# Performance work log

Measured on AMD Instinct MI355X. Metric: run time of the kernel, lower is better.

The kernel has to match this reference:

```python
import jax, jax.numpy as jnp
import numpy as np

B, N, Q, D = 1, 6, 10000, 256
HEADS, LEVELS, NPTS, ZANCH = 8, 1, 8, 4  # NPTS = 2*n_points, ZANCH = num_points_in_pillar
HF, WF = 32, 88
HD = D // HEADS


def setup_inputs() -> dict:
    key = jax.random.key(0)
    ks = jax.random.split(key, 18)
    s = 1.0 / np.sqrt(D)
    inp = {
        'queries': jax.random.normal(ks[0], (B, N, Q, D), jnp.float32),
        'pos_emb': jax.random.normal(ks[1], (B, N, Q, D), jnp.float32),
        'lvl_emb': jax.random.normal(ks[2], (LEVELS, D), jnp.float32),
        'cam_emb': jax.random.normal(ks[3], (N, D), jnp.float32),
        'features0': jax.random.normal(ks[4], (B * N, D, HF, WF), jnp.float32),
        'reference_points_3D': jax.random.uniform(ks[5], (B, N, Q, ZANCH, 2), jnp.float32),
        'bev_mask': jax.random.randint(ks[6], (B, N, Q, ZANCH, 2), 0, 2).astype(bool),
        # MSDeformAttn3D params
        'W_value': jax.random.normal(ks[7], (D, D), jnp.float32) * s,
        'b_value': jnp.zeros((D,), jnp.float32),
        'W_off': jax.random.normal(ks[8], (HEADS * LEVELS * NPTS * 2, D), jnp.float32) * 0.01,
        'b_off': jax.random.uniform(ks[9], (HEADS * LEVELS * NPTS * 2,), jnp.float32, -2.0, 2.0),
        'W_attn': jax.random.normal(ks[10], (HEADS * LEVELS * NPTS, D), jnp.float32) * s,
        'b_attn': jnp.zeros((HEADS * LEVELS * NPTS,), jnp.float32),
        'W_inner': jax.random.normal(ks[11], (D, D), jnp.float32) * s,
        'b_inner': jnp.zeros((D,), jnp.float32),
        # SpatialCrossAttention.output_proj
        'W_out': jax.random.normal(ks[12], (D, D), jnp.float32) * s,
        'b_out': jnp.zeros((D,), jnp.float32),
    }
    return inp


def _bilinear(value_t, loc, H, W):
    # value_t: (bn, heads, H*W, hd); loc: (bn, q, heads, pts, 2) normalized to [0,1]
    bn, q, heads, pts, _ = loc.shape
    hd = value_t.shape[-1]
    # grid_sample(2*loc-1, align_corners=False) -> pixel coord = loc*size - 0.5
    x = loc[..., 0] * W - 0.5
    y = loc[..., 1] * H - 0.5
    x0 = jnp.floor(x); y0 = jnp.floor(y)
    dx = x - x0; dy = y - y0
    x0 = x0.astype(jnp.int32); y0 = y0.astype(jnp.int32)
    out = jnp.zeros((bn, heads, q * pts, hd), value_t.dtype)
    corners = ((0, 0, (1 - dx) * (1 - dy)), (1, 0, dx * (1 - dy)),
               (0, 1, (1 - dx) * dy), (1, 1, dx * dy))
    for ox, oy, w in corners:
        xi = x0 + ox; yi = y0 + oy
        valid = (xi >= 0) & (xi < W) & (yi >= 0) & (yi < H)  # zero padding
        wgt = jnp.where(valid, w, 0.0)
        idx = jnp.clip(yi, 0, H - 1) * W + jnp.clip(xi, 0, W - 1)  # (bn,q,heads,pts)
        idx_t = idx.transpose(0, 2, 1, 3).reshape(bn, heads, q * pts)
        g = jnp.take_along_axis(value_t, idx_t[..., None], axis=2)  # (bn,heads,q*pts,hd)
        wgt_t = wgt.transpose(0, 2, 1, 3).reshape(bn, heads, q * pts)
        out = out + g * wgt_t[..., None]
    return out.reshape(bn, heads, q, pts, hd)


def _forward(queries, pos_emb, lvl_emb, cam_emb, features0, reference_points_3D, bev_mask,
             W_value, b_value, W_off, b_off, W_attn, b_attn, W_inner, b_inner, W_out, b_out):
    b, n, q, d = queries.shape
    hf, wf = features0.shape[-2:]
    # flatten features + level/cam embeddings -> (b*n, hw, d)
    feat = features0.reshape(b, n, d, hf * wf)
    feat = feat + lvl_emb[0][None, None, :, None] + cam_emb[None, :, :, None]
    input_flatten = feat.transpose(0, 1, 3, 2).reshape(b * n, hf * wf, d)

    qp = (queries + pos_emb).reshape(b * n, q, d)
    ref = reference_points_3D.reshape(b * n, q, ZANCH, 2)

    # --- MSDeformAttn3D (single level) ---
    value = (input_flatten @ W_value.T + b_value).reshape(b * n, hf * wf, HEADS, HD)
    off = (qp @ W_off.T + b_off).reshape(b * n, q, HEADS, LEVELS, NPTS, 2)
    attw = jax.nn.softmax((qp @ W_attn.T + b_attn).reshape(b * n, q, HEADS, LEVELS * NPTS), axis=-1)
    attw = attw.reshape(b * n, q, HEADS, LEVELS, NPTS)
    normalizer = jnp.array([wf, hf], queries.dtype)  # (W, H)
    pts_per_z = NPTS // ZANCH
    off_z = off.reshape(b * n, q, HEADS, LEVELS, pts_per_z, ZANCH, 2)
    loc = ref[:, :, None, None, None, :, :] + off_z / normalizer
    loc = loc.reshape(b * n, q, HEADS, LEVELS, NPTS, 2)

    value_t = value.transpose(0, 2, 1, 3)  # (bn, heads, hw, hd)
    sampled = _bilinear(value_t, loc[:, :, :, 0], hf, wf)  # (bn,heads,q,pts,hd)
    attw_t = attw[:, :, :, 0].transpose(0, 2, 1, 3)  # (bn,heads,q,pts)
    out = jnp.einsum('bhqp,bhqpc->bqhc', attw_t, sampled).reshape(b * n, q, d)
    out = out @ W_inner.T + b_inner

    # --- scatter back per camera, normalize by hit count ---
    attn = out.reshape(b, n, q, d)
    # indexes come from batch 0's mask (as in the original code)
    hit = (bev_mask[0, :, :, :, 0].astype(jnp.int32).sum(-1) > 0).astype(queries.dtype)  # (n,q)
    slots = (attn * hit[None, :, :, None]).sum(1)  # (b,q,d)
    count = (bev_mask[..., 0].astype(jnp.int32).sum(-1) > 0).astype(queries.dtype).sum(1)
    count = jnp.clip(count, 1.0, None)  # (b,q)
    slots = slots / count[..., None]
    return slots @ W_out.T + b_out


def reference(queries, pos_emb, lvl_emb, cam_emb, features0, reference_points_3D, bev_mask,
              W_value, b_value, W_off, b_off, W_attn, b_attn, W_inner, b_inner, W_out, b_out):
    return _forward(queries, pos_emb, lvl_emb, cam_emb, features0, reference_points_3D, bev_mask,
                    W_value, b_value, W_off, b_off, W_attn, b_attn, W_inner, b_inner, W_out, b_out)
```

## Files before the change

### kernel.cpp

```cpp
#include <hip/hip_runtime.h>
#include <hip/hip_bf16.h>

#define BN     6
#define NQ     10000
#define DIM    256
#define HEADS  8
#define HDD    32
#define HF_    32
#define WF_    88
#define HW_    (HF_*WF_)
#define MTOT   (BN*NQ)

typedef __attribute__((ext_vector_type(8))) unsigned short ushort8_t;
typedef __attribute__((ext_vector_type(8))) short bf16x8;
typedef __attribute__((ext_vector_type(4))) float f32x4;

static __device__ inline unsigned short f2bf(float x) {
    __hip_bfloat16 b = __float2bfloat16(x);
    return *(unsigned short*)&b;
}

__global__ __launch_bounds__(256)
void k_wcvt(const float* __restrict__ Wv, const float* __restrict__ Wo,
            const float* __restrict__ Wa, const float* __restrict__ Wi,
            const float* __restrict__ Wz,
            unsigned short* __restrict__ Wv_bf, unsigned short* __restrict__ Woa_bf,
            unsigned short* __restrict__ Wi_bf, unsigned short* __restrict__ Wz_bf)
{
    const int i4 = (blockIdx.x*256 + threadIdx.x) * 4;
    if (i4 < 65536) {
        float4 v;
        ushort4 p;
        v = *(const float4*)(Wv+i4); p.x=f2bf(v.x);p.y=f2bf(v.y);p.z=f2bf(v.z);p.w=f2bf(v.w);
        *(ushort4*)(Wv_bf+i4) = p;
        v = *(const float4*)(Wi+i4); p.x=f2bf(v.x);p.y=f2bf(v.y);p.z=f2bf(v.z);p.w=f2bf(v.w);
        *(ushort4*)(Wi_bf+i4) = p;
        v = *(const float4*)(Wz+i4); p.x=f2bf(v.x);p.y=f2bf(v.y);p.z=f2bf(v.z);p.w=f2bf(v.w);
        *(ushort4*)(Wz_bf+i4) = p;
    }
    if (i4 < 32768) {
        float4 v = *(const float4*)(Wo+i4);
        ushort4 p; p.x=f2bf(v.x);p.y=f2bf(v.y);p.z=f2bf(v.z);p.w=f2bf(v.w);
        *(ushort4*)(Woa_bf+i4) = p;
    }
    if (i4 < 16384) {
        float4 v = *(const float4*)(Wa+i4);
        ushort4 p; p.x=f2bf(v.x);p.y=f2bf(v.y);p.z=f2bf(v.z);p.w=f2bf(v.w);
        *(ushort4*)(Woa_bf+32768+i4) = p;
    }
}

__global__ __launch_bounds__(256)
void k_ebias(const float* __restrict__ lvl, const float* __restrict__ cam,
             const float* __restrict__ Wv, const float* __restrict__ bv,
             float* __restrict__ ebias)
{
    const int n = blockIdx.x;
    const int j = threadIdx.x;
    __shared__ float e[DIM];
    e[j] = lvl[j] + cam[n*DIM + j];
    __syncthreads();
    const float* w = Wv + (size_t)j*DIM;
    float s = bv[j];
    for (int d = 0; d < DIM; ++d) s += e[d]*w[d];
    ebias[n*DIM + j] = s;
}

__global__ __launch_bounds__(256)
void k_mask(const int* __restrict__ bev, float* __restrict__ hitf,
            float* __restrict__ scale, float* __restrict__ biasf)
{
    const int q = blockIdx.x*256 + threadIdx.x;
    if (q >= NQ) return;
    float cnt = 0.f;
    #pragma unroll
    for (int n = 0; n < BN; ++n) {
        int hit = 0;
        #pragma unroll
        for (int z = 0; z < 4; ++z)
            hit |= (bev[(((size_t)n*NQ + q)*4 + z)*2] != 0);
        hitf[(size_t)n*NQ + q] = (float)hit;
        cnt += (float)hit;
    }
    biasf[q] = (cnt > 0.f) ? 1.f : 0.f;
    scale[q] = 1.f / fmaxf(cnt, 1.f);
}

__global__ __launch_bounds__(256)
void k_feat(const float* __restrict__ feat, unsigned short* __restrict__ featT)
{
    __shared__ float Tf[64][68];
    const int cam = blockIdx.z;
    const int d0 = blockIdx.y * 64;
    const int p0 = blockIdx.x * 64;
    const int tid = threadIdx.x;
    #pragma unroll
    for (int i = 0; i < 4; ++i) {
        const int d = (tid>>4) + i*16;
        const int p4 = (tid&15)*4;
        *(float4*)&Tf[d][p4] = *(const float4*)(feat + ((size_t)cam*DIM + d0 + d)*HW_ + p0 + p4);
    }
    __syncthreads();
    const int p = tid>>2, dq = tid&3;
    unsigned short* ob = featT + ((size_t)cam*HW_ + p0 + p)*DIM + d0;
    #pragma unroll
    for (int i = 0; i < 4; ++i) {
        const int d4 = dq*4 + i*16;
        ushort4 pk;
        pk.x = f2bf(Tf[d4+0][p]); pk.y = f2bf(Tf[d4+1][p]);
        pk.z = f2bf(Tf[d4+2][p]); pk.w = f2bf(Tf[d4+3][p]);
        *(ushort4*)(ob + d4) = pk;
    }
}

__global__ __launch_bounds__(256)
void k_value_mfma(const unsigned short* __restrict__ featT,
                  const unsigned short* __restrict__ Wv_bf,
                  const float* __restrict__ ebias,
                  unsigned short* __restrict__ value_bf)
{
    __shared__ unsigned short Ap[128][72];
    __shared__ unsigned short Bc[64][72];
    const int cam = blockIdx.z;
    const int p0 = blockIdx.x * 128;
    const int c0 = blockIdx.y * 64;
    const int tid = threadIdx.x;
    const int lane = tid & 63, wave = tid >> 6;
    const int quad = lane >> 4, l15 = lane & 15;
    f32x4 acc[2][4] = {};
    const unsigned short* fbase = featT + ((size_t)cam*HW_ + p0)*DIM;

    for (int k0 = 0; k0 < DIM; k0 += 64) {
        #pragma unroll
        for (int i = 0; i < 4; ++i) {
            const int row = (tid>>3) + i*32;
            const int k8 = (tid&7)*8;
            *(ushort8_t*)&Ap[row][k8] = *(const ushort8_t*)(fbase + (size_t)row*DIM + k0 + k8);
        }
        #pragma unroll
        for (int i = 0; i < 2; ++i) {
            const int row = (tid>>3) + i*32;
            const int k8 = (tid&7)*8;
            *(ushort8_t*)&Bc[row][k8] = *(const ushort8_t*)(Wv_bf + (size_t)(c0+row)*DIM + k0 + k8);
        }
        __syncthreads();
        #pragma unroll
        for (int s = 0; s < 2; ++s) {
            const int kf = s*32 + quad*8;
            bf16x8 a[2], b[4];
            #pragma unroll
            for (int mt = 0; mt < 2; ++mt)
                a[mt] = *(const bf16x8*)&Ap[(wave*2+mt)*16 + l15][kf];
            #pragma unroll
            for (int nt = 0; nt < 4; ++nt)
                b[nt] = *(const bf16x8*)&Bc[nt*16 + l15][kf];
            #pragma unroll
            for (int mt = 0; mt < 2; ++mt)
                #pragma unroll
                for (int nt = 0; nt < 4; ++nt)
                    acc[mt][nt] = __builtin_amdgcn_mfma_f32_16x16x32_bf16(a[mt], b[nt], acc[mt][nt], 0,0,0);
        }
        __syncthreads();
    }
    #pragma unroll
    for (int nt = 0; nt < 4; ++nt) {
        const int c = c0 + nt*16 + l15;
        const float eb = ebias[cam*DIM + c];
        const int h = c >> 5, cc = c & 31;
        unsigned short* vb = value_bf + (size_t)(cam*HEADS + h)*HW_*HDD + cc;
        #pragma unroll
        for (int mt = 0; mt < 2; ++mt)
            #pragma unroll
            for (int r = 0; r < 4; ++r) {
                const int p = p0 + (wave*2+mt)*16 + quad*4 + r;
                vb[(size_t)p*HDD] = f2bf(acc[mt][nt][r] + eb);
            }
    }
}

__global__ __launch_bounds__(256, 3)
void k_offattn(const float* __restrict__ Qr, const float* __restrict__ Pe,
               const unsigned short* __restrict__ Woa_bf,
               const float* __restrict__ boff, const float* __restrict__ battn,
               float* __restrict__ off_ws, float* __restrict__ attw_ws)
{
    __shared__ char smraw[32*204*4];
    unsigned short (*A_lds)[264] = (unsigned short (*)[264])smraw;
    float (*C_lds)[204] = (float (*)[204])smraw;

    const int m0 = blockIdx.x * 32;
    const int tid = threadIdx.x;
    const int lane = tid & 63, wave = tid >> 6;
    const int quad = lane >> 4, l15 = lane & 15;
    const int n0 = wave * 48;

    bf16x8 breg[3][8];
    #pragma unroll
    for (int nt = 0; nt < 3; ++nt) {
        const unsigned short* wb = Woa_bf + (size_t)(n0 + nt*16 + l15)*DIM + quad*8;
        #pragma unroll
        for (int kc = 0; kc < 8; ++kc)
            breg[nt][kc] = *(const bf16x8*)(wb + kc*32);
    }

    {
        const int row = tid >> 3;
        const int c8  = tid & 7;
        const float* qb = Qr + (size_t)(m0 + row)*DIM;
        const float* pb = Pe + (size_t)(m0 + row)*DIM;
        #pragma unroll
        for (int j = 0; j < 8; ++j) {
            const int col = c8*4 + j*32;
            const float4 x = *(const float4*)(qb + col);
            const float4 y = *(const float4*)(pb + col);
            ushort4 pk;
            pk.x = f2bf(x.x+y.x); pk.y = f2bf(x.y+y.y);
            pk.z = f2bf(x.z+y.z); pk.w = f2bf(x.w+y.w);
            *(ushort4*)&A_lds[row][col] = pk;
        }
    }
    __syncthreads();

    f32x4 acc[2][3] = {};
    #pragma unroll
    for (int kc = 0; kc < 8; ++kc) {
        const int kk = kc*32 + quad*8;
        const bf16x8 a0 = *(const bf16x8*)&A_lds[l15][kk];
        const bf16x8 a1 = *(const bf16x8*)&A_lds[16 + l15][kk];
        #pragma unroll
        for (int nt = 0; nt < 3; ++nt) {
            acc[0][nt] = __builtin_amdgcn_mfma_f32_16x16x32_bf16(a0, breg[nt][kc], acc[0][nt], 0,0,0);
            acc[1][nt] = __builtin_amdgcn_mfma_f32_16x16x32_bf16(a1, breg[nt][kc], acc[1][nt], 0,0,0);
        }
    }

    __syncthreads();
    #pragma unroll
    for (int nt = 0; nt < 3; ++nt) {
        const int col = n0 + nt*16 + l15;
        const float bias = (col < 128) ? boff[col] : battn[col-128];
        #pragma unroll
        for (int mt = 0; mt < 2; ++mt) {
            #pragma unroll
            for (int r = 0; r < 4; ++r)
                C_lds[mt*16 + quad*4 + r][col] = acc[mt][nt][r] + bias;
        }
    }
    __syncthreads();
    #pragma unroll
    for (int i = 0; i < 4; ++i) {
        const int idx = i*256 + tid;
        const int row = idx >> 5, c4 = (idx & 31)*4;
        *(float4*)(off_ws + ((size_t)(m0+row))*128 + c4) = *(float4*)&C_lds[row][c4];
    }
    #pragma unroll
    for (int i = 0; i < 2; ++i) {
        const int idx = i*256 + tid;
        const int row = idx >> 4, c4 = (idx & 15)*4;
        *(float4*)(attw_ws + ((size_t)(m0+row))*64 + c4) = *(float4*)&C_lds[row][128 + c4];
    }
}

__global__ __launch_bounds__(256)
void k_sample(const unsigned short* __restrict__ value_bf,
              const float* __restrict__ off_ws, const float* __restrict__ attw_ws,
              const float* __restrict__ ref3d, const float* __restrict__ hitf,
              const float* __restrict__ scale, unsigned short* __restrict__ asum_bf)
{
    const int q0 = blockIdx.x * 8;
    const int tid = threadIdx.x;

    __shared__ float s_off[8][128];
    __shared__ float s_att[8][64];
    __shared__ float s_ref[8][8];
    __shared__ float s_hit[BN][8];
    __shared__ float s_scl[8];

    if (tid < 48) s_hit[tid>>3][tid&7] = hitf[(size_t)(tid>>3)*NQ + q0 + (tid&7)];
    if (tid < 8)  s_scl[tid] = scale[q0 + tid];

    const int quarter = tid & 3;
    const int h  = (tid >> 2) & 7;
    const int ql = tid >> 5;

    float acc[8];
    #pragma unroll
    for (int c = 0; c < 8; ++c) acc[c] = 0.f;

    for (int n = 0; n < BN; ++n) {
        __syncthreads();
        {
            const float4* so = (const float4*)(off_ws + ((size_t)n*NQ + q0)*128);
            ((float4*)&s_off[0][0])[tid] = so[tid];
            const float2* sa = (const float2*)(attw_ws + ((size_t)n*NQ + q0)*64);
            ((float2*)&s_att[0][0])[tid] = sa[tid];
            if (tid < 64)
                (&s_ref[0][0])[tid] = (ref3d + ((size_t)n*NQ + q0)*8)[tid];
        }
        __syncthreads();

        if (s_hit[n][ql] != 0.f) {
            float lg[8];
            float mx = -1e30f;
            #pragma unroll
            for (int p = 0; p < 8; ++p) { lg[p] = s_att[ql][h*8+p]; mx = fmaxf(mx, lg[p]); }
            float ssum = 0.f;
            #pragma unroll
            for (int p = 0; p < 8; ++p) { lg[p] = __expf(lg[p]-mx); ssum += lg[p]; }
            const float inv = 1.f/ssum;

            const unsigned short* vbase =
                value_bf + (size_t)(n*HEADS + h)*HW_*HDD + quarter*8;

            #pragma unroll
            for (int p = 0; p < 8; ++p) {
                const int z = p & 3;
                const float ax = s_ref[ql][z*2+0]*WF_ + s_off[ql][h*16+p*2+0] - 0.5f;
                const float ay = s_ref[ql][z*2+1]*HF_ + s_off[ql][h*16+p*2+1] - 0.5f;
                const float fx = floorf(ax), fy = floorf(ay);
                const float dx = ax-fx, dy = ay-fy;
                const int x0 = (int)fx, y0 = (int)fy;
                const float wp = lg[p]*inv;
                #pragma unroll
                for (int oy = 0; oy < 2; ++oy) {
                    const int yi = y0 + oy;
                    const float wy = oy ? dy : 1.f-dy;
                    #pragma unroll
                    for (int ox = 0; ox < 2; ++ox) {
                        const int xi = x0 + ox;
                        const float wx = ox ? dx : 1.f-dx;
                        const bool valid = ((unsigned)xi < WF_) & ((unsigned)yi < HF_);
                        const float cw = valid ? wp*wy*wx : 0.f;
                        const int xc = min(max(xi, 0), WF_-1);
                        const int yc = min(max(yi, 0), HF_-1);
                        const ushort8_t v = *(const ushort8_t*)(vbase + (size_t)(yc*WF_ + xc)*HDD);
                        #pragma unroll
                        for (int c = 0; c < 8; ++c)
                            acc[c] += cw * __uint_as_float(((unsigned)v[c]) << 16);
                    }
                }
            }
        }
    }

    const float sc = s_scl[ql];
    ushort8_t o;
    #pragma unroll
    for (int c = 0; c < 8; ++c) o[c] = f2bf(acc[c]*sc);
    *(ushort8_t*)(asum_bf + ((size_t)(q0+ql))*DIM + h*HDD + quarter*8) = o;
}

__global__ __launch_bounds__(256)
void k_gemm_mfma(const unsigned short* __restrict__ A_bf,
                 const unsigned short* __restrict__ W_bf,
                 const float* __restrict__ bias, const float* __restrict__ rowscale,
                 float* __restrict__ out_f, unsigned short* __restrict__ out_b, int M)
{
    __shared__ unsigned short As[128][72];
    __shared__ unsigned short Bs[64][72];
    const int m0 = blockIdx.x * 128;
    const int j0 = blockIdx.y * 64;
    const int tid = threadIdx.x;
    const int lane = tid & 63, wave = tid >> 6;
    const int quad = lane >> 4, l15 = lane & 15;
    f32x4 acc[2][4] = {};

    for (int k0 = 0; k0 < DIM; k0 += 64) {
        #pragma unroll
        for (int i = 0; i < 4; ++i) {
            const int row = (tid>>3) + i*32;
            const int k8 = (tid&7)*8;
            ushort8_t v = {0,0,0,0,0,0,0,0};
            if (m0 + row < M)
                v = *(const ushort8_t*)(A_bf + (size_t)(m0+row)*DIM + k0 + k8);
            *(ushort8_t*)&As[row][k8] = v;
        }
        #pragma unroll
        for (int i = 0; i < 2; ++i) {
            const int row = (tid>>3) + i*32;
            const int k8 = (tid&7)*8;
            *(ushort8_t*)&Bs[row][k8] = *(const ushort8_t*)(W_bf + (size_t)(j0+row)*DIM + k0 + k8);
        }
        __syncthreads();
        #pragma unroll
        for (int s = 0; s < 2; ++s) {
            const int kf = s*32 + quad*8;
            bf16x8 a[2], b[4];
            #pragma unroll
            for (int mt = 0; mt < 2; ++mt)
                a[mt] = *(const bf16x8*)&As[(wave*2+mt)*16 + l15][kf];
            #pragma unroll
            for (int nt = 0; nt < 4; ++nt)
                b[nt] = *(const bf16x8*)&Bs[nt*16 + l15][kf];
            #pragma unroll
            for (int mt = 0; mt < 2; ++mt)
                #pragma unroll
                for (int nt = 0; nt < 4; ++nt)
                    acc[mt][nt] = __builtin_amdgcn_mfma_f32_16x16x32_bf16(a[mt], b[nt], acc[mt][nt], 0,0,0);
        }
        __syncthreads();
    }
    #pragma unroll
    for (int nt = 0; nt < 4; ++nt) {
        const int j = j0 + nt*16 + l15;
        const float bj = bias[j];
        #pragma unroll
        for (int mt = 0; mt < 2; ++mt) {
            #pragma unroll
            for (int r = 0; r < 4; ++r) {
                const int m = m0 + (wave*2+mt)*16 + quad*4 + r;
                if (m >= M) continue;
                const float f = rowscale ? rowscale[m] : 1.f;
                const float v = acc[mt][nt][r] + f*bj;
                if (out_f) out_f[(size_t)m*DIM + j] = v;
                if (out_b) out_b[(size_t)m*DIM + j] = f2bf(v);
            }
        }
    }
}

extern "C" void kernel_launch(void* const* d_in, const int* in_sizes, int n_in,
                              void* d_out, int out_size, void* d_ws, size_t ws_size,
                              hipStream_t stream)
{
    const float* queries = (const float*)d_in[0];
    const float* pos_emb = (const float*)d_in[1];
    const float* lvl_emb = (const float*)d_in[2];
    const float* cam_emb = (const float*)d_in[3];
    const float* features= (const float*)d_in[4];
    const float* ref3d   = (const float*)d_in[5];
    const int*   bev     = (const int*)d_in[6];
    const float* Wv = (const float*)d_in[7];
    const float* bv = (const float*)d_in[8];
    const float* Wo = (const float*)d_in[9];
    const float* bo = (const float*)d_in[10];
    const float* Wa = (const float*)d_in[11];
    const float* ba = (const float*)d_in[12];
    const float* Wi = (const float*)d_in[13];
    const float* bi = (const float*)d_in[14];
    const float* Wz = (const float*)d_in[15];
    const float* bz = (const float*)d_in[16];
    float* out = (float*)d_out;

    char* ws = (char*)d_ws;
    size_t o = 0;
    auto alloc = [&](size_t bytes) { char* p = ws + o; o += (bytes + 255) & ~size_t(255); return p; };
    unsigned short* value_bf = (unsigned short*)alloc((size_t)BN*HEADS*HW_*HDD*2);
    unsigned short* featT    = (unsigned short*)alloc((size_t)BN*HW_*DIM*2);
    float* off_ws   = (float*)alloc((size_t)MTOT*128*4);
    float* attw_ws  = (float*)alloc((size_t)MTOT*64*4);
    unsigned short* asum_bf  = (unsigned short*)alloc((size_t)NQ*DIM*2);
    unsigned short* slots_bf = (unsigned short*)alloc((size_t)NQ*DIM*2);
    unsigned short* Wv_bf  = (unsigned short*)alloc(65536*2);
    unsigned short* Woa_bf = (unsigned short*)alloc(49152*2);
    unsigned short* Wi_bf  = (unsigned short*)alloc(65536*2);
    unsigned short* Wz_bf  = (unsigned short*)alloc(65536*2);
    float* hitf   = (float*)alloc((size_t)BN*NQ*4);
    float* scalev = (float*)alloc(NQ*4);
    float* biasf  = (float*)alloc(NQ*4);
    float* ebias  = (float*)alloc(BN*DIM*4);

    k_wcvt  <<<64, 256, 0, stream>>>(Wv, Wo, Wa, Wi, Wz, Wv_bf, Woa_bf, Wi_bf, Wz_bf);
    k_ebias <<<BN, 256, 0, stream>>>(lvl_emb, cam_emb, Wv, bv, ebias);
    k_mask  <<<(NQ+255)/256, 256, 0, stream>>>(bev, hitf, scalev, biasf);
    k_feat  <<<dim3(HW_/64, DIM/64, BN), 256, 0, stream>>>(features, featT);
    k_value_mfma<<<dim3(HW_/128, DIM/64, BN), 256, 0, stream>>>(featT, Wv_bf, ebias, value_bf);
    k_offattn<<<MTOT/32, 256, 0, stream>>>(queries, pos_emb, Woa_bf, bo, ba, off_ws, attw_ws);
    k_sample <<<NQ/8, 256, 0, stream>>>(value_bf, off_ws, attw_ws, ref3d, hitf, scalev, asum_bf);
    k_gemm_mfma<<<dim3((NQ+127)/128, DIM/64), 256, 0, stream>>>(asum_bf, Wi_bf, bi, biasf, nullptr, slots_bf, NQ);
    k_gemm_mfma<<<dim3((NQ+127)/128, DIM/64), 256, 0, stream>>>(slots_bf, Wz_bf, bz, nullptr, out, nullptr, NQ);
}
```

Before: 331.2 us.

## Move softmax into offset GEMM epilogue and halve sampling threads per head

The softmax over attention logits moves out of the sampling kernel into the epilogue of the offset/attention projection kernel, so it runs once per query-camera-head instead of being repeated by four threads. The sampling kernel now uses 128 threads, each handling 16 channels with two 16-byte loads per corner, which halves the redundant per-thread coordinate and weight computation. The trade-off is fewer threads per block, less parallelism for hiding gather latency, and more registers per thread.

```diff
diff --git a/kernel.cpp b/kernel.cpp
--- a/kernel.cpp
+++ b/kernel.cpp
@@ -247,6 +247,20 @@
         }
     }
     __syncthreads();
+    {
+        float* a = &C_lds[tid>>3][128 + (tid&7)*8];
+        float lg[8];
+        float mx = -1e30f;
+        #pragma unroll
+        for (int p = 0; p < 8; ++p) { lg[p] = a[p]; mx = fmaxf(mx, lg[p]); }
+        float ssum = 0.f;
+        #pragma unroll
+        for (int p = 0; p < 8; ++p) { lg[p] = __expf(lg[p]-mx); ssum += lg[p]; }
+        const float inv = 1.f/ssum;
+        #pragma unroll
+        for (int p = 0; p < 8; ++p) a[p] = lg[p]*inv;
+    }
+    __syncthreads();
     #pragma unroll
     for (int i = 0; i < 4; ++i) {
         const int idx = i*256 + tid;
@@ -261,7 +275,7 @@
     }
 }
 
-__global__ __launch_bounds__(256)
+__global__ __launch_bounds__(128)
 void k_sample(const unsigned short* __restrict__ value_bf,
               const float* __restrict__ off_ws, const float* __restrict__ attw_ws,
               const float* __restrict__ ref3d, const float* __restrict__ hitf,
@@ -279,48 +293,40 @@
     if (tid < 48) s_hit[tid>>3][tid&7] = hitf[(size_t)(tid>>3)*NQ + q0 + (tid&7)];
     if (tid < 8)  s_scl[tid] = scale[q0 + tid];
 
-    const int quarter = tid & 3;
-    const int h  = (tid >> 2) & 7;
-    const int ql = tid >> 5;
-
-    float acc[8];
-    #pragma unroll
-    for (int c = 0; c < 8; ++c) acc[c] = 0.f;
+    const int half = tid & 1;
+    const int h    = (tid >> 1) & 7;
+    const int ql   = tid >> 4;
+
+    float acc[16];
+    #pragma unroll
+    for (int c = 0; c < 16; ++c) acc[c] = 0.f;
 
     for (int n = 0; n < BN; ++n) {
         __syncthreads();
         {
             const float4* so = (const float4*)(off_ws + ((size_t)n*NQ + q0)*128);
-            ((float4*)&s_off[0][0])[tid] = so[tid];
-            const float2* sa = (const float2*)(attw_ws + ((size_t)n*NQ + q0)*64);
-            ((float2*)&s_att[0][0])[tid] = sa[tid];
+            ((float4*)&s_off[0][0])[tid]       = so[tid];
+            ((float4*)&s_off[0][0])[tid + 128] = so[tid + 128];
+            const float4* sa = (const float4*)(attw_ws + ((size_t)n*NQ + q0)*64);
+            ((float4*)&s_att[0][0])[tid] = sa[tid];
             if (tid < 64)
                 (&s_ref[0][0])[tid] = (ref3d + ((size_t)n*NQ + q0)*8)[tid];
         }
         __syncthreads();
 
         if (s_hit[n][ql] != 0.f) {
-            float lg[8];
-            float mx = -1e30f;
-            #pragma unroll
-            for (int p = 0; p < 8; ++p) { lg[p] = s_att[ql][h*8+p]; mx = fmaxf(mx, lg[p]); }
-            float ssum = 0.f;
-            #pragma unroll
-            for (int p = 0; p < 8; ++p) { lg[p] = __expf(lg[p]-mx); ssum += lg[p]; }
-            const float inv = 1.f/ssum;
-
             const unsigned short* vbase =
-                value_bf + (size_t)(n*HEADS + h)*HW_*HDD + quarter*8;
+                value_bf + (size_t)(n*HEADS + h)*HW_*HDD + half*16;
 
             #pragma unroll
             for (int p = 0; p < 8; ++p) {
                 const int z = p & 3;
+                const float wp = s_att[ql][h*8+p];
                 const float ax = s_ref[ql][z*2+0]*WF_ + s_off[ql][h*16+p*2+0] - 0.5f;
                 const float ay = s_ref[ql][z*2+1]*HF_ + s_off[ql][h*16+p*2+1] - 0.5f;
                 const float fx = floorf(ax), fy = floorf(ay);
                 const float dx = ax-fx, dy = ay-fy;
                 const int x0 = (int)fx, y0 = (int)fy;
-                const float wp = lg[p]*inv;
                 #pragma unroll
                 for (int oy = 0; oy < 2; ++oy) {
                     const int yi = y0 + oy;
@@ -333,10 +339,14 @@
                         const float cw = valid ? wp*wy*wx : 0.f;
                         const int xc = min(max(xi, 0), WF_-1);
                         const int yc = min(max(yi, 0), HF_-1);
-                        const ushort8_t v = *(const ushort8_t*)(vbase + (size_t)(yc*WF_ + xc)*HDD);
+                        const unsigned short* vp = vbase + (size_t)(yc*WF_ + xc)*HDD;
+                        const ushort8_t v0 = *(const ushort8_t*)(vp);
+                        const ushort8_t v1 = *(const ushort8_t*)(vp + 8);
                         #pragma unroll
-                        for (int c = 0; c < 8; ++c)
-                            acc[c] += cw * __uint_as_float(((unsigned)v[c]) << 16);
+                        for (int c = 0; c < 8; ++c) {
+                            acc[c]   += cw * __uint_as_float(((unsigned)v0[c]) << 16);
+                            acc[8+c] += cw * __uint_as_float(((unsigned)v1[c]) << 16);
+                        }
                     }
                 }
             }
@@ -344,10 +354,14 @@
     }
 
     const float sc = s_scl[ql];
+    unsigned short* ob = asum_bf + ((size_t)(q0+ql))*DIM + h*HDD + half*16;
     ushort8_t o;
     #pragma unroll
     for (int c = 0; c < 8; ++c) o[c] = f2bf(acc[c]*sc);
-    *(ushort8_t*)(asum_bf + ((size_t)(q0+ql))*DIM + h*HDD + quarter*8) = o;
+    *(ushort8_t*)(ob) = o;
+    #pragma unroll
+    for (int c = 0; c < 8; ++c) o[c] = f2bf(acc[8+c]*sc);
+    *(ushort8_t*)(ob + 8) = o;
 }
 
 __global__ __launch_bounds__(256)
@@ -466,7 +480,7 @@
     k_feat  <<<dim3(HW_/64, DIM/64, BN), 256, 0, stream>>>(features, featT);
     k_value_mfma<<<dim3(HW_/128, DIM/64, BN), 256, 0, stream>>>(featT, Wv_bf, ebias, value_bf);
     k_offattn<<<MTOT/32, 256, 0, stream>>>(queries, pos_emb, Woa_bf, bo, ba, off_ws, attw_ws);
-    k_sample <<<NQ/8, 256, 0, stream>>>(value_bf, off_ws, attw_ws, ref3d, hitf, scalev, asum_bf);
+    k_sample <<<NQ/8, 128, 0, stream>>>(value_bf, off_ws, attw_ws, ref3d, hitf, scalev, asum_bf);
     k_gemm_mfma<<<dim3((NQ+127)/128, DIM/64), 256, 0, stream>>>(asum_bf, Wi_bf, bi, biasf, nullptr, slots_bf, NQ);
     k_gemm_mfma<<<dim3((NQ+127)/128, DIM/64), 256, 0, stream>>>(slots_bf, Wz_bf, bz, nullptr, out, nullptr, NQ);
 }
```

Result: slower. 381.8 us (+15.3%).
